# Performance work log

Measured on AMD Instinct MI355X. Metric: run time of the kernel, lower is better.

Reference implementation:

```python
import jax, jax.numpy as jnp
import numpy as np

B, N, D, H_IMG, W_IMG = 1, 6, 128, 28, 60
HB, WB = 50, 50
HEADS, DH = 4, 32
INNER = HEADS * DH  # 128 == D
Q = HB * WB
NK = N * H_IMG * W_IMG


def _ln(x, w, b, eps=1e-5):
    m = jnp.mean(x, axis=-1, keepdims=True)
    v = jnp.var(x, axis=-1, keepdims=True)
    return (x - m) * jax.lax.rsqrt(v + eps) * w + b


def setup_inputs() -> dict:
    key = jax.random.key(0)
    ks = jax.random.split(key, 20)
    s = 0.02
    inp = {
        "q": jax.random.normal(ks[0], (B, D, HB, WB), jnp.float32),
        "k": jax.random.normal(ks[1], (B, N, D, H_IMG, W_IMG), jnp.float32),
        "v": jax.random.normal(ks[2], (B, N, D, H_IMG, W_IMG), jnp.float32),
        "W_logits": jax.random.uniform(ks[3], (B, Q, NK), jnp.float32),
        "vis_flat": jax.random.randint(ks[4], (B, Q, NK), 0, 2).astype(jnp.int32),
        "skip": jax.random.normal(ks[5], (B, D, HB, WB), jnp.float32),
        # LayerNorm params
        "qn_w": jnp.ones((D,), jnp.float32), "qn_b": jnp.zeros((D,), jnp.float32),
        "kn_w": jnp.ones((D,), jnp.float32), "kn_b": jnp.zeros((D,), jnp.float32),
        "vn_w": jnp.ones((D,), jnp.float32), "vn_b": jnp.zeros((D,), jnp.float32),
        "pre_w": jnp.ones((D,), jnp.float32), "pre_b": jnp.zeros((D,), jnp.float32),
        "post_w": jnp.ones((D,), jnp.float32), "post_b": jnp.zeros((D,), jnp.float32),
        # Linear params, stored [in, out]
        "wq": jax.random.normal(ks[6], (D, INNER), jnp.float32) * s,
        "bq": jnp.zeros((INNER,), jnp.float32),
        "wk": jax.random.normal(ks[7], (D, INNER), jnp.float32) * s,
        "bk": jnp.zeros((INNER,), jnp.float32),
        "wv": jax.random.normal(ks[8], (D, INNER), jnp.float32) * s,
        "bv": jnp.zeros((INNER,), jnp.float32),
        "wp": jax.random.normal(ks[9], (INNER, D), jnp.float32) * s,
        "bp": jnp.zeros((D,), jnp.float32),
        "w1": jax.random.normal(ks[10], (D, 2 * D), jnp.float32) * s,
        "b1": jnp.zeros((2 * D,), jnp.float32),
        "w2": jax.random.normal(ks[11], (2 * D, D), jnp.float32) * s,
        "b2": jnp.zeros((D,), jnp.float32),
    }
    return inp


def reference(q, k, v, W_logits, vis_flat, skip,
              qn_w, qn_b, kn_w, kn_b, vn_w, vn_b, pre_w, pre_b, post_w, post_b,
              wq, bq, wk, bk, wv, bv, wp, bp, w1, b1, w2, b2):
    b, d, Hb, Wb = q.shape
    _, n, _, hi, wi = k.shape
    Qn = Hb * Wb
    # b d H W -> b (H W) d ; b n d h w -> b (n h w) d
    qf = q.reshape(b, d, Qn).transpose(0, 2, 1)
    kf = k.transpose(0, 1, 3, 4, 2).reshape(b, n * hi * wi, d)
    vf = v.transpose(0, 1, 3, 4, 2).reshape(b, n * hi * wi, d)
    qf = _ln(qf, qn_w, qn_b)
    kf = _ln(kf, kn_w, kn_b)
    vf = _ln(vf, vn_w, vn_b)
    qh = (qf @ wq + bq).reshape(b, Qn, HEADS, DH).transpose(0, 2, 1, 3)
    kh = (kf @ wk + bk).reshape(b, -1, HEADS, DH).transpose(0, 2, 1, 3)
    vh = (vf @ wv + bv).reshape(b, -1, HEADS, DH).transpose(0, 2, 1, 3)
    scale = DH ** (-0.5)
    logits = jnp.einsum('bhqd,bhkd->bhqk', qh, kh) * scale  # [b,h,Q,NK]
    neg_inf = jnp.finfo(logits.dtype).min
    logits = jnp.where(vis_flat[:, None] == 0, neg_inf, logits)
    logits = logits * W_logits[:, None]  # multiplicative EAF weighting
    attn = jax.nn.softmax(logits, axis=-1)
    out = jnp.einsum('bhqk,bhkd->bhqd', attn, vh)
    out = out.transpose(0, 2, 1, 3).reshape(b, Qn, INNER)
    out = out @ wp + bp
    z = out + skip.reshape(b, d, Qn).transpose(0, 2, 1)
    z = _ln(z, pre_w, pre_b)
    z = z + (jax.nn.gelu(z @ w1 + b1, approximate=False) @ w2 + b2)
    z = _ln(z, post_w, post_b)
    return z.transpose(0, 2, 1).reshape(b, d, Hb, Wb)
```

## Files before the change

### kernel.cpp

```cpp
#include <hip/hip_runtime.h>
#include <hip/hip_bf16.h>
#include <math.h>

typedef short short8 __attribute__((ext_vector_type(8)));
typedef float floatx4 __attribute__((ext_vector_type(4)));
typedef int   intx4  __attribute__((ext_vector_type(4)));

#define D 128
#define Q 2500
#define QPAD 2560
#define NK 10080
#define NKPAD 10112
#define SPLITS 21
#define CPS 15
#define OPS 163904
#define LPS 10304
#define QSCALE 0.25501268426834347f
#define NEGBIG -3.0e38f

__device__ __forceinline__ unsigned short f2bf(float f) {
    unsigned u = __float_as_uint(f);
    unsigned r = (u + 0x7fffu + ((u >> 16) & 1u)) >> 16;
    return (unsigned short)r;
}
__device__ __forceinline__ unsigned pack2bf(float lo, float hi) {
    unsigned u0 = __float_as_uint(lo) + 0x8000u;
    unsigned u1 = __float_as_uint(hi) + 0x8000u;
    return (u0 >> 16) | (u1 & 0xffff0000u);
}
__device__ __forceinline__ float bflo(unsigned u) { return __uint_as_float(u << 16); }
__device__ __forceinline__ float bfhi(unsigned u) { return __uint_as_float(u & 0xffff0000u); }

__global__ void wcvt_kernel(const float* __restrict__ wq, const float* __restrict__ wk,
                            const float* __restrict__ wv, const float* __restrict__ wp,
                            const float* __restrict__ w1, const float* __restrict__ w2,
                            unsigned short* __restrict__ wqT, unsigned short* __restrict__ wkT,
                            unsigned short* __restrict__ wvT, unsigned short* __restrict__ wpT,
                            unsigned short* __restrict__ w1T, unsigned short* __restrict__ w2T) {
    int idx = blockIdx.x * 256 + threadIdx.x;
    if (idx < 49152) {
        int m = idx >> 14;
        int local = idx & 16383;
        int n = local >> 7, kk = local & 127;
        const float* w = (m == 0) ? wq : ((m == 1) ? wk : wv);
        unsigned short* o = (m == 0) ? wqT : ((m == 1) ? wkT : wvT);
        o[local] = f2bf(w[kk * 128 + n]);
    } else if (idx < 65536) {
        int local = idx - 49152;
        int n = local >> 7, kk = local & 127;
        wpT[local] = f2bf(wp[kk * 128 + n]);
    } else if (idx < 98304) {
        int local = idx - 65536;
        int n = local >> 7, kk = local & 127;
        w1T[local] = f2bf(w1[kk * 256 + n]);
    } else {
        int local = idx - 98304;
        int n = local >> 8, kk = local & 255;
        w2T[local] = f2bf(w2[kk * 128 + n]);
    }
}

__global__ __launch_bounds__(256) void ln_kernel(
    const float* __restrict__ qi, const float* __restrict__ ki, const float* __restrict__ vi,
    const float* __restrict__ qw, const float* __restrict__ qb,
    const float* __restrict__ kw, const float* __restrict__ kb,
    const float* __restrict__ vw, const float* __restrict__ vb,
    unsigned short* __restrict__ xq, unsigned short* __restrict__ xk,
    unsigned short* __restrict__ xv) {
    __shared__ float lds[16 * 132];
    int bid = blockIdx.x, t = threadIdx.x;
    const float* src; unsigned short* dst; const float *g, *b;
    int S, valid;
    if (bid < 157) {
        int p0 = bid * 16;
        src = qi + p0; S = Q; dst = xq + p0 * D; g = qw; b = qb;
        valid = Q - p0; if (valid > 16) valid = 16;
    } else if (bid < 787) {
        int tt = bid - 157;
        int n = tt / 105, r = (tt - n * 105) * 16;
        src = ki + (size_t)(n * 128) * 1680 + r; S = 1680;
        dst = xk + (n * 1680 + r) * D; g = kw; b = kb; valid = 16;
    } else {
        int tt = bid - 787;
        int n = tt / 105, r = (tt - n * 105) * 16;
        src = vi + (size_t)(n * 128) * 1680 + r; S = 1680;
        dst = xv + (n * 1680 + r) * D; g = vw; b = vb; valid = 16;
    }
    int c4 = t & 3, d = t >> 2;
    floatx4 fa = {0.f, 0.f, 0.f, 0.f}, fb = {0.f, 0.f, 0.f, 0.f};
    if (c4 * 4 < valid) {
        fa = *(const floatx4*)(src + d * S + c4 * 4);
        fb = *(const floatx4*)(src + (d + 64) * S + c4 * 4);
    }
    #pragma unroll
    for (int j = 0; j < 4; j++) {
        lds[(c4 * 4 + j) * 132 + d] = fa[j];
        lds[(c4 * 4 + j) * 132 + d + 64] = fb[j];
    }
    __syncthreads();
    int lane = t & 63, wv = t >> 6;
    int pos = wv * 4 + (lane >> 4), l15 = lane & 15;
    floatx4 xa = *(const floatx4*)(&lds[pos * 132 + l15 * 8]);
    floatx4 xb = *(const floatx4*)(&lds[pos * 132 + l15 * 8 + 4]);
    float s = 0.f, ss = 0.f;
    #pragma unroll
    for (int j = 0; j < 4; j++) { s += xa[j] + xb[j]; ss += xa[j] * xa[j] + xb[j] * xb[j]; }
    #pragma unroll
    for (int m = 1; m <= 8; m <<= 1) { s += __shfl_xor(s, m, 64); ss += __shfl_xor(ss, m, 64); }
    float mean = s * (1.0f / 128.0f);
    float var = ss * (1.0f / 128.0f) - mean * mean;
    float rstd = rsqrtf(var + 1e-5f);
    floatx4 g0 = *(const floatx4*)(g + l15 * 8), g1 = *(const floatx4*)(g + l15 * 8 + 4);
    floatx4 b0 = *(const floatx4*)(b + l15 * 8), b1 = *(const floatx4*)(b + l15 * 8 + 4);
    short8 o;
    #pragma unroll
    for (int j = 0; j < 4; j++) {
        o[j] = (short)f2bf((xa[j] - mean) * rstd * g0[j] + b0[j]);
        o[4 + j] = (short)f2bf((xb[j] - mean) * rstd * g1[j] + b1[j]);
    }
    if (pos < valid) *(short8*)(dst + pos * D + l15 * 8) = o;
}

__global__ __launch_bounds__(256) void proj_kernel(
    const unsigned short* __restrict__ xq, const unsigned short* __restrict__ xk,
    const unsigned short* __restrict__ xv,
    const unsigned short* __restrict__ wqT, const unsigned short* __restrict__ wkT,
    const unsigned short* __restrict__ wvT,
    const float* __restrict__ bq, const float* __restrict__ bk, const float* __restrict__ bv,
    unsigned short* __restrict__ qh, unsigned short* __restrict__ kh,
    unsigned short* __restrict__ vhT) {
    __shared__ short vlds[128 * 72];
    int bid = blockIdx.x;
    const unsigned short *src, *wT; const float* bias; int mb, mode; float scale;
    if (bid < 40)       { mode = 0; src = xq; wT = wqT; bias = bq; mb = bid * 64; scale = QSCALE; }
    else if (bid < 198) { mode = 1; src = xk; wT = wkT; bias = bk; mb = (bid - 40) * 64; scale = 1.0f; }
    else                { mode = 2; src = xv; wT = wvT; bias = bv; mb = (bid - 198) * 64; scale = 1.0f; }
    int t = threadIdx.x, wave = t >> 6, lane = t & 63;
    int l15 = lane & 15, quad = lane >> 4;
    int m0 = mb + wave * 16;
    floatx4 acc[8];
    #pragma unroll
    for (int i = 0; i < 8; i++) acc[i] = (floatx4){0.f, 0.f, 0.f, 0.f};
    #pragma unroll
    for (int kf = 0; kf < 4; kf++) {
        short8 A = *(const short8*)(src + (m0 + l15) * D + kf * 32 + quad * 8);
        #pragma unroll
        for (int nt = 0; nt < 8; nt++) {
            short8 Bv = *(const short8*)(wT + (nt * 16 + l15) * D + kf * 32 + quad * 8);
            acc[nt] = __builtin_amdgcn_mfma_f32_16x16x32_bf16(A, Bv, acc[nt], 0, 0, 0);
        }
    }
    if (mode != 2) {
        unsigned short* dst = (mode == 0) ? qh : kh;
        #pragma unroll
        for (int nt = 0; nt < 8; nt++) {
            float bb = bias[nt * 16 + l15];
            #pragma unroll
            for (int r = 0; r < 4; r++)
                dst[(m0 + quad * 4 + r) * D + nt * 16 + l15] = f2bf((acc[nt][r] + bb) * scale);
        }
    } else {
        #pragma unroll
        for (int nt = 0; nt < 8; nt++) {
            float bb = bias[nt * 16 + l15];
            #pragma unroll
            for (int r = 0; r < 4; r++)
                vlds[(nt * 16 + l15) * 72 + (wave * 16 + quad * 4 + r)] =
                    (short)f2bf(acc[nt][r] + bb);
        }
        __syncthreads();
        int pr = t & 31, dd = t >> 5;
        int sub = pr >> 4, i = pr & 15;
        #pragma unroll
        for (int pass = 0; pass < 16; pass++) {
            int d = pass * 8 + dd;
            unsigned lo = (unsigned short)vlds[d * 72 + sub * 32 + i];
            unsigned hi = (unsigned short)vlds[d * 72 + sub * 32 + 16 + i];
            *(unsigned*)(vhT + (size_t)d * NKPAD + mb + sub * 32 + 2 * i) = lo | (hi << 16);
        }
    }
}

__global__ __launch_bounds__(256, 3) void attn_kernel(
    const unsigned short* __restrict__ qh, const unsigned short* __restrict__ kh,
    const unsigned short* __restrict__ vhT,
    const float* __restrict__ Wl, const int* __restrict__ vis,
    unsigned* __restrict__ OpartU, float* __restrict__ lpart) {
    int bid = blockIdx.x;
    int split = bid % SPLITS, qt4 = bid / SPLITS;
    int lane = threadIdx.x & 63, wave = threadIdx.x >> 6;
    int l15 = lane & 15, quad = lane >> 4;
    int qb = (qt4 * 4 + wave) * 16;
    int k00 = split * (CPS * 32);

    short8 qB[4];
    #pragma unroll
    for (int h = 0; h < 4; h++)
        qB[h] = *(const short8*)(qh + (qb + l15) * D + h * 32 + quad * 8);

    int wrow = qb + l15; if (wrow >= Q) wrow = Q - 1;
    const float* wp = Wl + (size_t)wrow * NK + k00 + quad * 4;
    const int*   vp = vis + (size_t)wrow * NK + k00 + quad * 4;

    const floatx4 zf = {0.f, 0.f, 0.f, 0.f};
    floatx4 O[4][2];
    float lacc[4];
    #pragma unroll
    for (int h = 0; h < 4; h++) { O[h][0] = zf; O[h][1] = zf; lacc[h] = 0.f; }

    int sidx[4];
    #pragma unroll
    for (int jj = 0; jj < 4; jj++)
        sidx[jj] = l15 + 16 * ((quad & 1) * 2 + (jj >> 1));
    bool hiTile = quad >= 2;

    floatx4 wc0 = *(const floatx4*)(wp);
    floatx4 wc1 = *(const floatx4*)(wp + 16);
    intx4   vc0 = *(const intx4*)(vp);
    intx4   vc1 = *(const intx4*)(vp + 16);

    #pragma unroll 1
    for (int c = 0; c < CPS; c++) {
        int k0 = k00 + c * 32;
        floatx4 wn0, wn1; intx4 vn0, vn1;
        if (c + 1 < CPS) {
            wn0 = *(const floatx4*)(wp + (c + 1) * 32);
            wn1 = *(const floatx4*)(wp + (c + 1) * 32 + 16);
            vn0 = *(const intx4*)(vp + (c + 1) * 32);
            vn1 = *(const intx4*)(vp + (c + 1) * 32 + 16);
        }
        float a2[8], b2[8];
        #pragma unroll
        for (int r = 0; r < 4; r++) {
            a2[r]     = vc0[r] ? wc0[r] : 0.f;
            b2[r]     = vc0[r] ? 0.f : wc0[r] * NEGBIG;
            a2[4 + r] = vc1[r] ? wc1[r] : 0.f;
            b2[4 + r] = vc1[r] ? 0.f : wc1[r] * NEGBIG;
        }
        #pragma unroll
        for (int h = 0; h < 4; h++) {
            short8 kA0 = *(const short8*)(kh + (k0 + l15) * D + h * 32 + quad * 8);
            short8 kA1 = *(const short8*)(kh + (k0 + 16 + l15) * D + h * 32 + quad * 8);
            floatx4 S0 = __builtin_amdgcn_mfma_f32_16x16x32_bf16(kA0, qB[h], zf, 0, 0, 0);
            floatx4 S1 = __builtin_amdgcn_mfma_f32_16x16x32_bf16(kA1, qB[h], zf, 0, 0, 0);
            float p0[4], p1[4];
            #pragma unroll
            for (int r = 0; r < 4; r++) {
                p0[r] = exp2f(S0[r] * a2[r] + b2[r]);
                p1[r] = exp2f(S1[r] * a2[4 + r] + b2[4 + r]);
                lacc[h] += p0[r] + p1[r];
            }
            unsigned PP0[2] = {pack2bf(p0[0], p0[1]), pack2bf(p0[2], p0[3])};
            unsigned PP1[2] = {pack2bf(p1[0], p1[1]), pack2bf(p1[2], p1[3])};
            union { unsigned u[4]; short8 s; } pb;
            #pragma unroll
            for (int jj = 0; jj < 4; jj++) {
                unsigned s0 = (unsigned)__shfl((int)PP0[jj & 1], sidx[jj], 64);
                unsigned s1 = (unsigned)__shfl((int)PP1[jj & 1], sidx[jj], 64);
                pb.u[jj] = hiTile ? s1 : s0;
            }
            short8 vA0 = *(const short8*)(vhT + (size_t)(h * 32 + l15) * NKPAD + k0 + quad * 8);
            short8 vA1 = *(const short8*)(vhT + (size_t)(h * 32 + 16 + l15) * NKPAD + k0 + quad * 8);
            O[h][0] = __builtin_amdgcn_mfma_f32_16x16x32_bf16(vA0, pb.s, O[h][0], 0, 0, 0);
            O[h][1] = __builtin_amdgcn_mfma_f32_16x16x32_bf16(vA1, pb.s, O[h][1], 0, 0, 0);
        }
        wc0 = wn0; wc1 = wn1; vc0 = vn0; vc1 = vn1;
    }

    int row = qb + l15;
    #pragma unroll
    for (int h = 0; h < 4; h++) {
        float lv = lacc[h];
        lv += __shfl_xor(lv, 16, 64);
        lv += __shfl_xor(lv, 32, 64);
        if (quad == 0) lpart[(size_t)split * LPS + row * 4 + h] = lv;
        #pragma unroll
        for (int tl = 0; tl < 2; tl++) {
            uint2 o2;
            o2.x = pack2bf(O[h][tl][0], O[h][tl][1]);
            o2.y = pack2bf(O[h][tl][2], O[h][tl][3]);
            *(uint2*)(OpartU + (size_t)split * OPS + ((size_t)row * 4 + h) * 16 + tl * 8 + quad * 2) = o2;
        }
    }
}

__global__ void linv_kernel(const float* __restrict__ lpart, float* __restrict__ linv) {
    int i = blockIdx.x * 256 + threadIdx.x;
    float s = 0.f;
    #pragma unroll
    for (int sp = 0; sp < SPLITS; sp++) s += lpart[(size_t)sp * LPS + i];
    linv[i] = 1.0f / fmaxf(s, 1e-30f);
}

__global__ void combine_kernel(const unsigned* __restrict__ OpartU,
                               const float* __restrict__ linv,
                               unsigned* __restrict__ A1u) {
    int idx = blockIdx.x * 256 + threadIdx.x;
    float lo = 0.f, hi = 0.f;
    #pragma unroll
    for (int sp = 0; sp < SPLITS; sp++) {
        unsigned u = OpartU[(size_t)sp * OPS + idx];
        lo += bflo(u);
        hi += bfhi(u);
    }
    float inv = linv[idx >> 4];
    A1u[idx] = pack2bf(lo * inv, hi * inv);
}

__global__ __launch_bounds__(256) void mlp_kernel(
    const unsigned short* __restrict__ A1s, const unsigned short* __restrict__ wpT,
    const float* __restrict__ bp, const float* __restrict__ skip,
    const float* __restrict__ pre_w, const float* __restrict__ pre_b,
    const unsigned short* __restrict__ w1T, const float* __restrict__ b1,
    const unsigned short* __restrict__ w2T, const float* __restrict__ b2,
    const float* __restrict__ post_w, const float* __restrict__ post_b,
    float* __restrict__ out) {
    __shared__ __align__(16) char smem[51200];
    short* Z1 = (short*)smem;
    short* H1 = (short*)(smem + 17408);
    float* Zout = (float*)smem;

    int qb = blockIdx.x * 64;
    int t = threadIdx.x, wave = t >> 6, lane = t & 63;
    int l15 = lane & 15, quad = lane >> 4;
    int m0 = wave * 16;

    floatx4 z[8];
    #pragma unroll
    for (int i = 0; i < 8; i++) z[i] = (floatx4){0.f, 0.f, 0.f, 0.f};
    #pragma unroll
    for (int kf = 0; kf < 4; kf++) {
        short8 A = *(const short8*)(A1s + (qb + m0 + l15) * D + kf * 32 + quad * 8);
        #pragma unroll
        for (int nt = 0; nt < 8; nt++) {
            short8 Bv = *(const short8*)(wpT + (nt * 16 + l15) * D + kf * 32 + quad * 8);
            z[nt] = __builtin_amdgcn_mfma_f32_16x16x32_bf16(A, Bv, z[nt], 0, 0, 0);
        }
    }
    float Zv[8][4];
    #pragma unroll
    for (int nt = 0; nt < 8; nt++) {
        int n = nt * 16 + l15;
        float bb = bp[n];
        #pragma unroll
        for (int r = 0; r < 4; r++) {
            int q = qb + m0 + quad * 4 + r;
            int qc = q < Q ? q : (Q - 1);
            Zv[nt][r] = z[nt][r] + bb + skip[n * Q + qc];
        }
    }
    float Zn[8][4];
    {
        #pragma unroll
        for (int r = 0; r < 4; r++) {
            float s1 = 0.f, s2 = 0.f;
            #pragma unroll
            for (int nt = 0; nt < 8; nt++) { s1 += Zv[nt][r]; s2 += Zv[nt][r] * Zv[nt][r]; }
            #pragma unroll
            for (int m = 1; m <= 8; m <<= 1) { s1 += __shfl_xor(s1, m, 64); s2 += __shfl_xor(s2, m, 64); }
            float mean = s1 * (1.0f / 128.0f);
            float var = s2 * (1.0f / 128.0f) - mean * mean;
            float rstd = rsqrtf(var + 1e-5f);
            #pragma unroll
            for (int nt = 0; nt < 8; nt++) Zn[nt][r] = (Zv[nt][r] - mean) * rstd;
        }
        #pragma unroll
        for (int nt = 0; nt < 8; nt++) {
            int n = nt * 16 + l15;
            float g = pre_w[n], be = pre_b[n];
            #pragma unroll
            for (int r = 0; r < 4; r++) {
                Zn[nt][r] = Zn[nt][r] * g + be;
                Z1[(m0 + quad * 4 + r) * 136 + n] = (short)f2bf(Zn[nt][r]);
            }
        }
    }
    {
        floatx4 h2[16];
        #pragma unroll
        for (int i = 0; i < 16; i++) h2[i] = (floatx4){0.f, 0.f, 0.f, 0.f};
        #pragma unroll
        for (int kf = 0; kf < 4; kf++) {
            short8 A = *(const short8*)(Z1 + (m0 + l15) * 136 + kf * 32 + quad * 8);
            #pragma unroll
            for (int nt = 0; nt < 16; nt++) {
                short8 Bv = *(const short8*)(w1T + (nt * 16 + l15) * D + kf * 32 + quad * 8);
                h2[nt] = __builtin_amdgcn_mfma_f32_16x16x32_bf16(A, Bv, h2[nt], 0, 0, 0);
            }
        }
        #pragma unroll
        for (int nt = 0; nt < 16; nt++) {
            int n = nt * 16 + l15;
            float bb = b1[n];
            #pragma unroll
            for (int r = 0; r < 4; r++) {
                float x = h2[nt][r] + bb;
                float gl = 0.5f * x * (1.0f + erff(x * 0.70710678118654752f));
                H1[(m0 + quad * 4 + r) * 264 + n] = (short)f2bf(gl);
            }
        }
    }
    floatx4 o3[8];
    #pragma unroll
    for (int i = 0; i < 8; i++) o3[i] = (floatx4){0.f, 0.f, 0.f, 0.f};
    #pragma unroll
    for (int kf = 0; kf < 8; kf++) {
        short8 A = *(const short8*)(H1 + (m0 + l15) * 264 + kf * 32 + quad * 8);
        #pragma unroll
        for (int nt = 0; nt < 8; nt++) {
            short8 Bv = *(const short8*)(w2T + (nt * 16 + l15) * 256 + kf * 32 + quad * 8);
            o3[nt] = __builtin_amdgcn_mfma_f32_16x16x32_bf16(A, Bv, o3[nt], 0, 0, 0);
        }
    }
    float Z2[8][4];
    #pragma unroll
    for (int nt = 0; nt < 8; nt++) {
        int n = nt * 16 + l15;
        float bb = b2[n];
        #pragma unroll
        for (int r = 0; r < 4; r++) Z2[nt][r] = Zn[nt][r] + o3[nt][r] + bb;
    }
    float Zo[8][4];
    {
        #pragma unroll
        for (int r = 0; r < 4; r++) {
            float s1 = 0.f, s2 = 0.f;
            #pragma unroll
            for (int nt = 0; nt < 8; nt++) { s1 += Z2[nt][r]; s2 += Z2[nt][r] * Z2[nt][r]; }
            #pragma unroll
            for (int m = 1; m <= 8; m <<= 1) { s1 += __shfl_xor(s1, m, 64); s2 += __shfl_xor(s2, m, 64); }
            float mean = s1 * (1.0f / 128.0f);
            float var = s2 * (1.0f / 128.0f) - mean * mean;
            float rstd = rsqrtf(var + 1e-5f);
            #pragma unroll
            for (int nt = 0; nt < 8; nt++) Zo[nt][r] = (Z2[nt][r] - mean) * rstd;
        }
        #pragma unroll
        for (int nt = 0; nt < 8; nt++) {
            int n = nt * 16 + l15;
            float g = post_w[n], be = post_b[n];
            #pragma unroll
            for (int r = 0; r < 4; r++) Zo[nt][r] = Zo[nt][r] * g + be;
        }
    }
    __syncthreads();
    #pragma unroll
    for (int nt = 0; nt < 8; nt++)
        #pragma unroll
        for (int r = 0; r < 4; r++)
            Zout[(nt * 16 + l15) * 65 + m0 + quad * 4 + r] = Zo[nt][r];
    __syncthreads();
    {
        int pl = t & 63;
        int q = qb + pl;
        if (q < Q) {
            #pragma unroll
            for (int it = 0; it < 32; it++) {
                int n = it * 4 + (t >> 6);
                out[n * Q + q] = Zout[n * 65 + pl];
            }
        }
    }
}

extern "C" void kernel_launch(void* const* d_in, const int* in_sizes, int n_in,
                              void* d_out, int out_size, void* d_ws, size_t ws_size,
                              hipStream_t stream) {
    (void)in_sizes; (void)n_in; (void)out_size; (void)ws_size;
    const float* q      = (const float*)d_in[0];
    const float* k      = (const float*)d_in[1];
    const float* v      = (const float*)d_in[2];
    const float* Wl     = (const float*)d_in[3];
    const int*   vis    = (const int*)  d_in[4];
    const float* skip   = (const float*)d_in[5];
    const float* qn_w   = (const float*)d_in[6];
    const float* qn_b   = (const float*)d_in[7];
    const float* kn_w   = (const float*)d_in[8];
    const float* kn_b   = (const float*)d_in[9];
    const float* vn_w   = (const float*)d_in[10];
    const float* vn_b   = (const float*)d_in[11];
    const float* pre_w  = (const float*)d_in[12];
    const float* pre_b  = (const float*)d_in[13];
    const float* post_w = (const float*)d_in[14];
    const float* post_b = (const float*)d_in[15];
    const float* wq     = (const float*)d_in[16];
    const float* bq     = (const float*)d_in[17];
    const float* wk     = (const float*)d_in[18];
    const float* bk     = (const float*)d_in[19];
    const float* wv     = (const float*)d_in[20];
    const float* bv     = (const float*)d_in[21];
    const float* wp     = (const float*)d_in[22];
    const float* bp     = (const float*)d_in[23];
    const float* w1     = (const float*)d_in[24];
    const float* b1     = (const float*)d_in[25];
    const float* w2     = (const float*)d_in[26];
    const float* b2     = (const float*)d_in[27];
    float* out = (float*)d_out;

    char* ws = (char*)d_ws;
    unsigned short* xq  = (unsigned short*)(ws + 0);
    unsigned short* xk  = (unsigned short*)(ws + 655360);
    unsigned short* xv  = (unsigned short*)(ws + 3244032);
    unsigned short* qh  = (unsigned short*)(ws + 5832704);
    unsigned short* kh  = (unsigned short*)(ws + 6488064);
    unsigned short* vhT = (unsigned short*)(ws + 9076736);
    unsigned short* wqT = (unsigned short*)(ws + 11665408);
    unsigned short* wkT = (unsigned short*)(ws + 11698176);
    unsigned short* wvT = (unsigned short*)(ws + 11730944);
    unsigned short* wpT = (unsigned short*)(ws + 11763712);
    unsigned short* w1T = (unsigned short*)(ws + 11796480);
    unsigned short* w2T = (unsigned short*)(ws + 11862016);
    unsigned* OpartU    = (unsigned*)(ws + 11927552);
    float* lpart        = (float*)(ws + 25695488);
    float* linv         = (float*)(ws + 26561024);
    unsigned* A1u       = (unsigned*)(ws + 655360);

    wcvt_kernel<<<dim3(512), dim3(256), 0, stream>>>(wq, wk, wv, wp, w1, w2,
                                                     wqT, wkT, wvT, wpT, w1T, w2T);
    ln_kernel<<<dim3(1417), dim3(256), 0, stream>>>(q, k, v, qn_w, qn_b, kn_w, kn_b, vn_w, vn_b,
                                                    xq, xk, xv);
    proj_kernel<<<dim3(356), dim3(256), 0, stream>>>(xq, xk, xv, wqT, wkT, wvT, bq, bk, bv,
                                                     qh, kh, vhT);
    attn_kernel<<<dim3(40 * SPLITS), dim3(256), 0, stream>>>(qh, kh, vhT, Wl, vis, OpartU, lpart);
    linv_kernel<<<dim3(40), dim3(256), 0, stream>>>(lpart, linv);
    combine_kernel<<<dim3(640), dim3(256), 0, stream>>>(OpartU, linv, A1u);
    mlp_kernel<<<dim3(40), dim3(256), 0, stream>>>((const unsigned short*)A1u, wpT, bp, skip,
                                                   pre_w, pre_b, w1T, b1, w2T, b2,
                                                   post_w, post_b, out);
}
```

Measured before the change: 446.9 us.

## Stage K/V in LDS with double buffering, fuse prep and combine kernels, resplit attention

Attention blocks now cooperatively stage K and V chunks in double-buffered shared memory, and replace the shuffle-based P transpose with an LDS round trip. The split count goes from 21 to 35 with fewer chunks per split to raise parallelism. Weight conversion merges with the LayerNorm kernel, which now processes 32 positions per block. The linv and combine kernels are folded into the MLP kernel's prologue, cutting launches and an intermediate round trip, at the cost of more partial sums to reduce and extra barriers per chunk.

```diff
diff --git a/kernel.cpp b/kernel.cpp
--- a/kernel.cpp
+++ b/kernel.cpp
@@ -11,8 +11,8 @@
 #define QPAD 2560
 #define NK 10080
 #define NKPAD 10112
-#define SPLITS 21
-#define CPS 15
+#define SPLITS 35
+#define CPS 9
 #define OPS 163904
 #define LPS 10304
 #define QSCALE 0.25501268426834347f
@@ -31,94 +31,105 @@
 __device__ __forceinline__ float bflo(unsigned u) { return __uint_as_float(u << 16); }
 __device__ __forceinline__ float bfhi(unsigned u) { return __uint_as_float(u & 0xffff0000u); }
 
-__global__ void wcvt_kernel(const float* __restrict__ wq, const float* __restrict__ wk,
-                            const float* __restrict__ wv, const float* __restrict__ wp,
-                            const float* __restrict__ w1, const float* __restrict__ w2,
-                            unsigned short* __restrict__ wqT, unsigned short* __restrict__ wkT,
-                            unsigned short* __restrict__ wvT, unsigned short* __restrict__ wpT,
-                            unsigned short* __restrict__ w1T, unsigned short* __restrict__ w2T) {
-    int idx = blockIdx.x * 256 + threadIdx.x;
-    if (idx < 49152) {
-        int m = idx >> 14;
-        int local = idx & 16383;
-        int n = local >> 7, kk = local & 127;
-        const float* w = (m == 0) ? wq : ((m == 1) ? wk : wv);
-        unsigned short* o = (m == 0) ? wqT : ((m == 1) ? wkT : wvT);
-        o[local] = f2bf(w[kk * 128 + n]);
-    } else if (idx < 65536) {
-        int local = idx - 49152;
-        int n = local >> 7, kk = local & 127;
-        wpT[local] = f2bf(wp[kk * 128 + n]);
-    } else if (idx < 98304) {
-        int local = idx - 65536;
-        int n = local >> 7, kk = local & 127;
-        w1T[local] = f2bf(w1[kk * 256 + n]);
-    } else {
-        int local = idx - 98304;
-        int n = local >> 8, kk = local & 255;
-        w2T[local] = f2bf(w2[kk * 128 + n]);
-    }
-}
-
-__global__ __launch_bounds__(256) void ln_kernel(
+__global__ __launch_bounds__(256) void prep_kernel(
     const float* __restrict__ qi, const float* __restrict__ ki, const float* __restrict__ vi,
-    const float* __restrict__ qw, const float* __restrict__ qb,
+    const float* __restrict__ qw, const float* __restrict__ qb_,
     const float* __restrict__ kw, const float* __restrict__ kb,
     const float* __restrict__ vw, const float* __restrict__ vb,
     unsigned short* __restrict__ xq, unsigned short* __restrict__ xk,
-    unsigned short* __restrict__ xv) {
-    __shared__ float lds[16 * 132];
+    unsigned short* __restrict__ xv,
+    const float* __restrict__ wq, const float* __restrict__ wk,
+    const float* __restrict__ wv, const float* __restrict__ wp,
+    const float* __restrict__ w1, const float* __restrict__ w2,
+    unsigned short* __restrict__ wqT, unsigned short* __restrict__ wkT,
+    unsigned short* __restrict__ wvT, unsigned short* __restrict__ wpT,
+    unsigned short* __restrict__ w1T, unsigned short* __restrict__ w2T) {
     int bid = blockIdx.x, t = threadIdx.x;
+    if (bid >= 715) {
+        int idx = (bid - 715) * 256 + t;
+        if (idx < 49152) {
+            int m = idx >> 14;
+            int local = idx & 16383;
+            int n = local >> 7, kk = local & 127;
+            const float* w = (m == 0) ? wq : ((m == 1) ? wk : wv);
+            unsigned short* o = (m == 0) ? wqT : ((m == 1) ? wkT : wvT);
+            o[local] = f2bf(w[kk * 128 + n]);
+        } else if (idx < 65536) {
+            int local = idx - 49152;
+            int n = local >> 7, kk = local & 127;
+            wpT[local] = f2bf(wp[kk * 128 + n]);
+        } else if (idx < 98304) {
+            int local = idx - 65536;
+            int n = local >> 7, kk = local & 127;
+            w1T[local] = f2bf(w1[kk * 256 + n]);
+        } else {
+            int local = idx - 98304;
+            int n = local >> 8, kk = local & 255;
+            w2T[local] = f2bf(w2[kk * 128 + n]);
+        }
+        return;
+    }
+    __shared__ float lds2[32 * 132];
     const float* src; unsigned short* dst; const float *g, *b;
     int S, valid;
-    if (bid < 157) {
-        int p0 = bid * 16;
-        src = qi + p0; S = Q; dst = xq + p0 * D; g = qw; b = qb;
-        valid = Q - p0; if (valid > 16) valid = 16;
-    } else if (bid < 787) {
-        int tt = bid - 157;
-        int n = tt / 105, r = (tt - n * 105) * 16;
+    if (bid < 79) {
+        int p0 = bid * 32;
+        src = qi + p0; S = Q; dst = xq + p0 * D; g = qw; b = qb_;
+        valid = Q - p0; if (valid > 32) valid = 32;
+    } else if (bid < 397) {
+        int tt = bid - 79;
+        int n = tt / 53, tile = tt - n * 53, r = tile * 32;
         src = ki + (size_t)(n * 128) * 1680 + r; S = 1680;
-        dst = xk + (n * 1680 + r) * D; g = kw; b = kb; valid = 16;
+        dst = xk + (n * 1680 + r) * D; g = kw; b = kb;
+        valid = 1680 - r; if (valid > 32) valid = 32;
     } else {
-        int tt = bid - 787;
-        int n = tt / 105, r = (tt - n * 105) * 16;
+        int tt = bid - 397;
+        int n = tt / 53, tile = tt - n * 53, r = tile * 32;
         src = vi + (size_t)(n * 128) * 1680 + r; S = 1680;
-        dst = xv + (n * 1680 + r) * D; g = vw; b = vb; valid = 16;
-    }
-    int c4 = t & 3, d = t >> 2;
-    floatx4 fa = {0.f, 0.f, 0.f, 0.f}, fb = {0.f, 0.f, 0.f, 0.f};
-    if (c4 * 4 < valid) {
-        fa = *(const floatx4*)(src + d * S + c4 * 4);
-        fb = *(const floatx4*)(src + (d + 64) * S + c4 * 4);
-    }
-    #pragma unroll
-    for (int j = 0; j < 4; j++) {
-        lds[(c4 * 4 + j) * 132 + d] = fa[j];
-        lds[(c4 * 4 + j) * 132 + d + 64] = fb[j];
+        dst = xv + (n * 1680 + r) * D; g = vw; b = vb;
+        valid = 1680 - r; if (valid > 32) valid = 32;
+    }
+    #pragma unroll
+    for (int pass = 0; pass < 4; pass++) {
+        int s = pass * 256 + t;
+        int d = s >> 3, ps = s & 7;
+        floatx4 val = {0.f, 0.f, 0.f, 0.f};
+        if (ps * 4 < valid) val = *(const floatx4*)(src + (size_t)d * S + ps * 4);
+        #pragma unroll
+        for (int j = 0; j < 4; j++) lds2[(ps * 4 + j) * 132 + d] = val[j];
     }
     __syncthreads();
-    int lane = t & 63, wv = t >> 6;
-    int pos = wv * 4 + (lane >> 4), l15 = lane & 15;
-    floatx4 xa = *(const floatx4*)(&lds[pos * 132 + l15 * 8]);
-    floatx4 xb = *(const floatx4*)(&lds[pos * 132 + l15 * 8 + 4]);
+    int lane = t & 63, wvx = t >> 6;
+    int pos = wvx * 8 + (lane >> 3), l7 = lane & 7;
+    floatx4 x4[4];
+    #pragma unroll
+    for (int k = 0; k < 4; k++) x4[k] = *(const floatx4*)(&lds2[pos * 132 + l7 * 16 + k * 4]);
     float s = 0.f, ss = 0.f;
     #pragma unroll
-    for (int j = 0; j < 4; j++) { s += xa[j] + xb[j]; ss += xa[j] * xa[j] + xb[j] * xb[j]; }
-    #pragma unroll
-    for (int m = 1; m <= 8; m <<= 1) { s += __shfl_xor(s, m, 64); ss += __shfl_xor(ss, m, 64); }
+    for (int k = 0; k < 4; k++)
+        #pragma unroll
+        for (int j = 0; j < 4; j++) { s += x4[k][j]; ss += x4[k][j] * x4[k][j]; }
+    #pragma unroll
+    for (int m = 1; m <= 4; m <<= 1) { s += __shfl_xor(s, m, 64); ss += __shfl_xor(ss, m, 64); }
     float mean = s * (1.0f / 128.0f);
     float var = ss * (1.0f / 128.0f) - mean * mean;
     float rstd = rsqrtf(var + 1e-5f);
-    floatx4 g0 = *(const floatx4*)(g + l15 * 8), g1 = *(const floatx4*)(g + l15 * 8 + 4);
-    floatx4 b0 = *(const floatx4*)(b + l15 * 8), b1 = *(const floatx4*)(b + l15 * 8 + 4);
-    short8 o;
-    #pragma unroll
-    for (int j = 0; j < 4; j++) {
-        o[j] = (short)f2bf((xa[j] - mean) * rstd * g0[j] + b0[j]);
-        o[4 + j] = (short)f2bf((xb[j] - mean) * rstd * g1[j] + b1[j]);
-    }
-    if (pos < valid) *(short8*)(dst + pos * D + l15 * 8) = o;
+    short8 o1, o2;
+    #pragma unroll
+    for (int k = 0; k < 4; k++) {
+        floatx4 g4 = *(const floatx4*)(g + l7 * 16 + k * 4);
+        floatx4 b4 = *(const floatx4*)(b + l7 * 16 + k * 4);
+        #pragma unroll
+        for (int j = 0; j < 4; j++) {
+            float o = (x4[k][j] - mean) * rstd * g4[j] + b4[j];
+            if (k < 2) o1[k * 4 + j] = (short)f2bf(o);
+            else o2[(k - 2) * 4 + j] = (short)f2bf(o);
+        }
+    }
+    if (pos < valid) {
+        *(short8*)(dst + pos * D + l7 * 16) = o1;
+        *(short8*)(dst + pos * D + l7 * 16 + 8) = o2;
+    }
 }
 
 __global__ __launch_bounds__(256) void proj_kernel(
@@ -186,17 +197,27 @@
     const unsigned short* __restrict__ vhT,
     const float* __restrict__ Wl, const int* __restrict__ vis,
     unsigned* __restrict__ OpartU, float* __restrict__ lpart) {
+    __shared__ short Kl[2][32 * 136];
+    __shared__ short Vl[2][128 * 48];
+    __shared__ unsigned Pl[4][16 * 18];
     int bid = blockIdx.x;
-    int split = bid % SPLITS, qt4 = bid / SPLITS;
-    int lane = threadIdx.x & 63, wave = threadIdx.x >> 6;
+    int split = bid % SPLITS, qt = bid / SPLITS;
+    int t = threadIdx.x, wave = t >> 6, lane = t & 63;
     int l15 = lane & 15, quad = lane >> 4;
-    int qb = (qt4 * 4 + wave) * 16;
+    int qb = qt * 64 + wave * 16;
     int k00 = split * (CPS * 32);
 
     short8 qB[4];
     #pragma unroll
     for (int h = 0; h < 4; h++)
-        qB[h] = *(const short8*)(qh + (qb + l15) * D + h * 32 + quad * 8);
+        qB[h] = *(const short8*)(qh + (size_t)(qb + l15) * D + h * 32 + quad * 8);
+
+    int kr = t >> 3, ks = (t & 7) * 2;
+    int vd = t >> 1, vs = (t & 1) * 2;
+    const uint4* ksrc = (const uint4*)(kh + (size_t)(k00 + kr) * D + ks * 8);
+    const uint4* vsrc = (const uint4*)(vhT + (size_t)vd * NKPAD + k00 + vs * 8);
+    short* kdst = &Kl[0][kr * 136 + ks * 8];
+    short* vdst = &Vl[0][vd * 48 + vs * 8];
 
     int wrow = qb + l15; if (wrow >= Q) wrow = Q - 1;
     const float* wp = Wl + (size_t)wrow * NK + k00 + quad * 4;
@@ -208,22 +229,27 @@
     #pragma unroll
     for (int h = 0; h < 4; h++) { O[h][0] = zf; O[h][1] = zf; lacc[h] = 0.f; }
 
-    int sidx[4];
-    #pragma unroll
-    for (int jj = 0; jj < 4; jj++)
-        sidx[jj] = l15 + 16 * ((quad & 1) * 2 + (jj >> 1));
-    bool hiTile = quad >= 2;
-
-    floatx4 wc0 = *(const floatx4*)(wp);
+    uint4 ka = ksrc[0], kb2 = ksrc[1];
+    uint4 va = vsrc[0], vb2 = vsrc[1];
+    floatx4 wc0 = *(const floatx4*)wp;
     floatx4 wc1 = *(const floatx4*)(wp + 16);
-    intx4   vc0 = *(const intx4*)(vp);
-    intx4   vc1 = *(const intx4*)(vp + 16);
-
+    intx4 vc0 = *(const intx4*)vp;
+    intx4 vc1 = *(const intx4*)(vp + 16);
+    *(uint4*)kdst = ka;       *(uint4*)(kdst + 8) = kb2;
+    *(uint4*)vdst = va;       *(uint4*)(vdst + 8) = vb2;
+
+    unsigned* pw = Pl[wave];
     #pragma unroll 1
     for (int c = 0; c < CPS; c++) {
-        int k0 = k00 + c * 32;
+        __syncthreads();
+        int buf = c & 1;
+        uint4 nka, nkb, nva, nvb;
         floatx4 wn0, wn1; intx4 vn0, vn1;
         if (c + 1 < CPS) {
+            const uint4* ks2 = ksrc + (size_t)(c + 1) * 512;
+            const uint4* vs2 = vsrc + (size_t)(c + 1) * 4;
+            nka = ks2[0]; nkb = ks2[1];
+            nva = vs2[0]; nvb = vs2[1];
             wn0 = *(const floatx4*)(wp + (c + 1) * 32);
             wn1 = *(const floatx4*)(wp + (c + 1) * 32 + 16);
             vn0 = *(const intx4*)(vp + (c + 1) * 32);
@@ -237,10 +263,12 @@
             a2[4 + r] = vc1[r] ? wc1[r] : 0.f;
             b2[4 + r] = vc1[r] ? 0.f : wc1[r] * NEGBIG;
         }
+        const short* Kb = Kl[buf];
+        const short* Vb = Vl[buf];
         #pragma unroll
         for (int h = 0; h < 4; h++) {
-            short8 kA0 = *(const short8*)(kh + (k0 + l15) * D + h * 32 + quad * 8);
-            short8 kA1 = *(const short8*)(kh + (k0 + 16 + l15) * D + h * 32 + quad * 8);
+            short8 kA0 = *(const short8*)(Kb + l15 * 136 + h * 32 + quad * 8);
+            short8 kA1 = *(const short8*)(Kb + (16 + l15) * 136 + h * 32 + quad * 8);
             floatx4 S0 = __builtin_amdgcn_mfma_f32_16x16x32_bf16(kA0, qB[h], zf, 0, 0, 0);
             floatx4 S1 = __builtin_amdgcn_mfma_f32_16x16x32_bf16(kA1, qB[h], zf, 0, 0, 0);
             float p0[4], p1[4];
@@ -250,21 +278,26 @@
                 p1[r] = exp2f(S1[r] * a2[4 + r] + b2[4 + r]);
                 lacc[h] += p0[r] + p1[r];
             }
-            unsigned PP0[2] = {pack2bf(p0[0], p0[1]), pack2bf(p0[2], p0[3])};
-            unsigned PP1[2] = {pack2bf(p1[0], p1[1]), pack2bf(p1[2], p1[3])};
-            union { unsigned u[4]; short8 s; } pb;
-            #pragma unroll
-            for (int jj = 0; jj < 4; jj++) {
-                unsigned s0 = (unsigned)__shfl((int)PP0[jj & 1], sidx[jj], 64);
-                unsigned s1 = (unsigned)__shfl((int)PP1[jj & 1], sidx[jj], 64);
-                pb.u[jj] = hiTile ? s1 : s0;
-            }
-            short8 vA0 = *(const short8*)(vhT + (size_t)(h * 32 + l15) * NKPAD + k0 + quad * 8);
-            short8 vA1 = *(const short8*)(vhT + (size_t)(h * 32 + 16 + l15) * NKPAD + k0 + quad * 8);
-            O[h][0] = __builtin_amdgcn_mfma_f32_16x16x32_bf16(vA0, pb.s, O[h][0], 0, 0, 0);
-            O[h][1] = __builtin_amdgcn_mfma_f32_16x16x32_bf16(vA1, pb.s, O[h][1], 0, 0, 0);
-        }
-        wc0 = wn0; wc1 = wn1; vc0 = vn0; vc1 = vn1;
+            pw[(quad * 2) * 18 + l15]     = pack2bf(p0[0], p0[1]);
+            pw[(quad * 2 + 1) * 18 + l15] = pack2bf(p0[2], p0[3]);
+            pw[(8 + quad * 2) * 18 + l15]     = pack2bf(p1[0], p1[1]);
+            pw[(8 + quad * 2 + 1) * 18 + l15] = pack2bf(p1[2], p1[3]);
+            union { unsigned u[4]; short8 s8; } pb;
+            #pragma unroll
+            for (int jj = 0; jj < 4; jj++)
+                pb.u[jj] = pw[(quad * 4 + jj) * 18 + l15];
+            short8 vA0 = *(const short8*)(Vb + (h * 32 + l15) * 48 + quad * 8);
+            short8 vA1 = *(const short8*)(Vb + (h * 32 + 16 + l15) * 48 + quad * 8);
+            O[h][0] = __builtin_amdgcn_mfma_f32_16x16x32_bf16(vA0, pb.s8, O[h][0], 0, 0, 0);
+            O[h][1] = __builtin_amdgcn_mfma_f32_16x16x32_bf16(vA1, pb.s8, O[h][1], 0, 0, 0);
+        }
+        if (c + 1 < CPS) {
+            short* kd = buf ? kdst : (kdst + 32 * 136);
+            short* vd2 = buf ? vdst : (vdst + 128 * 48);
+            *(uint4*)kd = nka;       *(uint4*)(kd + 8) = nkb;
+            *(uint4*)vd2 = nva;      *(uint4*)(vd2 + 8) = nvb;
+            wc0 = wn0; wc1 = wn1; vc0 = vn0; vc1 = vn1;
+        }
     }
 
     int row = qb + l15;
@@ -284,53 +317,61 @@
     }
 }
 
-__global__ void linv_kernel(const float* __restrict__ lpart, float* __restrict__ linv) {
-    int i = blockIdx.x * 256 + threadIdx.x;
-    float s = 0.f;
-    #pragma unroll
-    for (int sp = 0; sp < SPLITS; sp++) s += lpart[(size_t)sp * LPS + i];
-    linv[i] = 1.0f / fmaxf(s, 1e-30f);
-}
-
-__global__ void combine_kernel(const unsigned* __restrict__ OpartU,
-                               const float* __restrict__ linv,
-                               unsigned* __restrict__ A1u) {
-    int idx = blockIdx.x * 256 + threadIdx.x;
-    float lo = 0.f, hi = 0.f;
-    #pragma unroll
-    for (int sp = 0; sp < SPLITS; sp++) {
-        unsigned u = OpartU[(size_t)sp * OPS + idx];
-        lo += bflo(u);
-        hi += bfhi(u);
-    }
-    float inv = linv[idx >> 4];
-    A1u[idx] = pack2bf(lo * inv, hi * inv);
-}
-
 __global__ __launch_bounds__(256) void mlp_kernel(
-    const unsigned short* __restrict__ A1s, const unsigned short* __restrict__ wpT,
+    const unsigned* __restrict__ Opart, const float* __restrict__ lpart,
+    const unsigned short* __restrict__ wpT,
     const float* __restrict__ bp, const float* __restrict__ skip,
     const float* __restrict__ pre_w, const float* __restrict__ pre_b,
     const unsigned short* __restrict__ w1T, const float* __restrict__ b1,
     const unsigned short* __restrict__ w2T, const float* __restrict__ b2,
     const float* __restrict__ post_w, const float* __restrict__ post_b,
     float* __restrict__ out) {
-    __shared__ __align__(16) char smem[51200];
-    short* Z1 = (short*)smem;
-    short* H1 = (short*)(smem + 17408);
-    float* Zout = (float*)smem;
+    __shared__ __align__(16) char smem[68608];
+    short* A1l = (short*)smem;
+    short* Z1 = (short*)(smem + 17408);
+    short* H1 = (short*)(smem + 34816);
+    float* Zout = (float*)(smem + 17408);
+    unsigned* A1u = (unsigned*)smem;
 
     int qb = blockIdx.x * 64;
     int t = threadIdx.x, wave = t >> 6, lane = t & 63;
     int l15 = lane & 15, quad = lane >> 4;
     int m0 = wave * 16;
 
+    {
+        int row = t >> 2, he = t & 3;
+        int grow = qb + row;
+        float lsum = 0.f;
+        #pragma unroll 5
+        for (int sp = 0; sp < SPLITS; sp++) lsum += lpart[(size_t)sp * LPS + grow * 4 + he];
+        float inv = 1.0f / fmaxf(lsum, 1e-30f);
+        size_t base = ((size_t)grow * 4 + he) * 16;
+        #pragma unroll
+        for (int sl = 0; sl < 4; sl++) {
+            float a0 = 0.f, a1 = 0.f, a2 = 0.f, a3 = 0.f, a4 = 0.f, a5 = 0.f, a6 = 0.f, a7 = 0.f;
+            #pragma unroll 5
+            for (int sp = 0; sp < SPLITS; sp++) {
+                uint4 u = *(const uint4*)(Opart + (size_t)sp * OPS + base + sl * 4);
+                a0 += bflo(u.x); a1 += bfhi(u.x);
+                a2 += bflo(u.y); a3 += bfhi(u.y);
+                a4 += bflo(u.z); a5 += bfhi(u.z);
+                a6 += bflo(u.w); a7 += bfhi(u.w);
+            }
+            int o = row * 68 + he * 16 + sl * 4;
+            A1u[o + 0] = pack2bf(a0 * inv, a1 * inv);
+            A1u[o + 1] = pack2bf(a2 * inv, a3 * inv);
+            A1u[o + 2] = pack2bf(a4 * inv, a5 * inv);
+            A1u[o + 3] = pack2bf(a6 * inv, a7 * inv);
+        }
+    }
+    __syncthreads();
+
     floatx4 z[8];
     #pragma unroll
     for (int i = 0; i < 8; i++) z[i] = (floatx4){0.f, 0.f, 0.f, 0.f};
     #pragma unroll
     for (int kf = 0; kf < 4; kf++) {
-        short8 A = *(const short8*)(A1s + (qb + m0 + l15) * D + kf * 32 + quad * 8);
+        short8 A = *(const short8*)(A1l + (m0 + l15) * 136 + kf * 32 + quad * 8);
         #pragma unroll
         for (int nt = 0; nt < 8; nt++) {
             short8 Bv = *(const short8*)(wpT + (nt * 16 + l15) * D + kf * 32 + quad * 8);
@@ -511,20 +552,15 @@
     unsigned short* w1T = (unsigned short*)(ws + 11796480);
     unsigned short* w2T = (unsigned short*)(ws + 11862016);
     unsigned* OpartU    = (unsigned*)(ws + 11927552);
-    float* lpart        = (float*)(ws + 25695488);
-    float* linv         = (float*)(ws + 26561024);
-    unsigned* A1u       = (unsigned*)(ws + 655360);
-
-    wcvt_kernel<<<dim3(512), dim3(256), 0, stream>>>(wq, wk, wv, wp, w1, w2,
-                                                     wqT, wkT, wvT, wpT, w1T, w2T);
-    ln_kernel<<<dim3(1417), dim3(256), 0, stream>>>(q, k, v, qn_w, qn_b, kn_w, kn_b, vn_w, vn_b,
-                                                    xq, xk, xv);
+    float* lpart        = (float*)(ws + 34874112);
+
+    prep_kernel<<<dim3(1227), dim3(256), 0, stream>>>(
+        q, k, v, qn_w, qn_b, kn_w, kn_b, vn_w, vn_b, xq, xk, xv,
+        wq, wk, wv, wp, w1, w2, wqT, wkT, wvT, wpT, w1T, w2T);
     proj_kernel<<<dim3(356), dim3(256), 0, stream>>>(xq, xk, xv, wqT, wkT, wvT, bq, bk, bv,
                                                      qh, kh, vhT);
     attn_kernel<<<dim3(40 * SPLITS), dim3(256), 0, stream>>>(qh, kh, vhT, Wl, vis, OpartU, lpart);
-    linv_kernel<<<dim3(40), dim3(256), 0, stream>>>(lpart, linv);
-    combine_kernel<<<dim3(640), dim3(256), 0, stream>>>(OpartU, linv, A1u);
-    mlp_kernel<<<dim3(40), dim3(256), 0, stream>>>((const unsigned short*)A1u, wpT, bp, skip,
+    mlp_kernel<<<dim3(40), dim3(256), 0, stream>>>(OpartU, lpart, wpT, bp, skip,
                                                    pre_w, pre_b, w1T, b1, w2T, b2,
                                                    post_w, post_b, out);
 }
```

New measurement: 365.7 us. 1.22x faster.
